# Kernel tuning notes

Measured on AMD Instinct MI355X. Metric: run time of the kernel, lower is better.

The kernel has to match this reference:

```python
import jax, jax.numpy as jnp
import numpy as np

D_MODEL = 1024
NHEAD = 16
HEAD_DIM = D_MODEL // NHEAD
SCALE = HEAD_DIM ** (-0.5)


def setup_inputs() -> dict:
    key = jax.random.key(0)
    k1, k2, k3 = jax.random.split(key, 3)
    B, T, C = 2, 2048, D_MODEL
    x = jax.random.normal(k1, (B, T, C), dtype=jnp.float32)
    W_qkv = jax.random.normal(k2, (3 * C, C), dtype=jnp.float32) * (C ** -0.5)
    b_qkv = jnp.zeros((3 * C,), dtype=jnp.float32)
    W_out = jax.random.normal(k3, (C, C), dtype=jnp.float32) * (C ** -0.5)
    b_out = jnp.zeros((C,), dtype=jnp.float32)
    return {"x": x, "W_qkv": W_qkv, "b_qkv": b_qkv, "W_out": W_out, "b_out": b_out}


def reference(x, W_qkv, b_qkv, W_out, b_out):
    B, T, C = x.shape
    H, hd = NHEAD, HEAD_DIM
    qkv = x @ W_qkv.T + b_qkv
    qkv = qkv.reshape(B, T, 3, H, hd).transpose(2, 0, 3, 1, 4)
    q, k, v = qkv[0], qkv[1], qkv[2]
    # scaled dot-product scores: (B,H,T,T)
    attn = jnp.einsum('bhqd,bhkd->bhqk', q, k) * SCALE
    # causal mask (is_causal=True): lower-triangular allowed
    causal = jnp.tril(jnp.ones((T, T), dtype=bool))
    attn = jnp.where(causal[None, None, :, :], attn, -jnp.inf)
    attn = jax.nn.softmax(attn, axis=-1)
    # (B,H,T,hd) -> (B,T,C)
    out = jnp.einsum('bhqk,bhkd->bhqd', attn, v)
    out = out.transpose(0, 2, 1, 3).reshape(B, T, C)
    out = out @ W_out.T + b_out
    return out
```

## Files before the change

### kernel.cpp

```cpp
#include <hip/hip_runtime.h>
#include <hip/hip_bf16.h>
#include <stdint.h>

#define D_MODEL 1024
#define NHEAD   16
#define HEAD_DIM 64
#define BATCH   2
#define SEQ     2048
#define M_TOK   (BATCH*SEQ)
#define N_QKV   (3*D_MODEL)
#define KDIM    1024
#define Q_SCALE (0.125f * 1.44269504088896f)

typedef __bf16 bf16_t;
typedef bf16_t bf16x8 __attribute__((ext_vector_type(8)));
typedef bf16_t bf16x4 __attribute__((ext_vector_type(4)));
typedef float  f32x4  __attribute__((ext_vector_type(4)));

__device__ __forceinline__ void gl_lds16(const void* g, void* l) {
    __builtin_amdgcn_global_load_lds(
        (__attribute__((address_space(1))) void*)(void*)(const_cast<void*>(g)),
        (__attribute__((address_space(3))) void*)l, 16, 0, 0);
}

#define N4_X  (M_TOK * KDIM / 4)
#define N4_W1 (N_QKV * KDIM / 4)
#define N4_W2 (D_MODEL * KDIM / 4)
__global__ void convert_all(const float* __restrict__ x,
                            const float* __restrict__ w1,
                            const float* __restrict__ w2,
                            bf16_t* __restrict__ ox,
                            bf16_t* __restrict__ o1,
                            bf16_t* __restrict__ o2) {
    int t = blockIdx.x * blockDim.x + threadIdx.x;
    const float* src;
    bf16_t* dst;
    int off;
    if (t < N4_X)                { src = x;  dst = ox; off = t; }
    else if (t < N4_X + N4_W1)   { src = w1; dst = o1; off = t - N4_X; }
    else                         { src = w2; dst = o2; off = t - N4_X - N4_W1; }
    float4 v = reinterpret_cast<const float4*>(src)[off];
    bf16x4 o = { (bf16_t)v.x, (bf16_t)v.y, (bf16_t)v.z, (bf16_t)v.w };
    reinterpret_cast<bf16x4*>(dst)[off] = o;
}

template <int MODE, int TN>
__global__ __launch_bounds__(256) void gemm_bt(
    const bf16_t* __restrict__ A,
    const bf16_t* __restrict__ Bw,
    const float*  __restrict__ bias,
    int N,
    bf16_t* __restrict__ qkv_out,
    bf16_t* __restrict__ vt_out,
    float*  __restrict__ f32_out)
{
    constexpr int NJ = TN / 32;
    __shared__ bf16_t As[128 * 64];
    __shared__ bf16_t Bs[TN * 64];

    const int cpx = gridDim.x >> 3;
    const int bid = (blockIdx.x & 7) * cpx + (blockIdx.x >> 3);

    const int nbn = N / TN;
    const int bm = bid / nbn;
    const int bn = bid % nbn;
    const int m0 = bm * 128, n0 = bn * TN;
    const int tid = threadIdx.x, wave = tid >> 6, lane = tid & 63;
    const int wr = wave >> 1, wc = wave & 1;

    f32x4 acc[4][NJ] = {};

    const int srow = lane >> 3;
    const int scol = ((lane & 7) ^ srow) * 8;
    const bf16_t* gA0 = A  + (size_t)(m0 + wave * 32 + srow) * KDIM + scol;
    const bf16_t* gB0 = Bw + (size_t)(n0 + wave * (TN / 4) + srow) * KDIM + scol;
    bf16_t* lA0 = &As[(wave * 32) * 64];
    bf16_t* lB0 = &Bs[(wave * (TN / 4)) * 64];

    const int fr = lane & 15;
    const int kq = lane >> 4;

    for (int k0 = 0; k0 < KDIM; k0 += 64) {
#pragma unroll
        for (int c = 0; c < 4; c++)
            gl_lds16(gA0 + (size_t)(c * 8) * KDIM + k0, lA0 + (c * 8) * 64);
#pragma unroll
        for (int c = 0; c < TN / 32; c++)
            gl_lds16(gB0 + (size_t)(c * 8) * KDIM + k0, lB0 + (c * 8) * 64);
        __syncthreads();

        bf16x8 af[2][4], bfr[2][NJ];
#pragma unroll
        for (int kk = 0; kk < 2; kk++) {
            const int ch = (((kk << 2) | kq) ^ (fr & 7)) * 8;
#pragma unroll
            for (int i = 0; i < 4; i++)
                af[kk][i] = *reinterpret_cast<const bf16x8*>(
                    &As[(wr * 64 + i * 16 + fr) * 64 + ch]);
#pragma unroll
            for (int j = 0; j < NJ; j++)
                bfr[kk][j] = *reinterpret_cast<const bf16x8*>(
                    &Bs[(wc * (TN / 2) + j * 16 + fr) * 64 + ch]);
        }
        __builtin_amdgcn_s_setprio(1);
#pragma unroll
        for (int i = 0; i < 4; i++)
#pragma unroll
            for (int j = 0; j < NJ; j++) {
                acc[i][j] = __builtin_amdgcn_mfma_f32_16x16x32_bf16(
                    af[0][i], bfr[0][j], acc[i][j], 0, 0, 0);
                acc[i][j] = __builtin_amdgcn_mfma_f32_16x16x32_bf16(
                    af[1][i], bfr[1][j], acc[i][j], 0, 0, 0);
            }
        __builtin_amdgcn_s_setprio(0);
        __syncthreads();
    }

#pragma unroll
    for (int i = 0; i < 4; i++) {
#pragma unroll
        for (int j = 0; j < NJ; j++) {
            const int col = n0 + wc * (TN / 2) + j * 16 + fr;
            const float bv = bias[col];
            const int row0 = m0 + wr * 64 + i * 16 + kq * 4;
            if (MODE == 1) {
#pragma unroll
                for (int r = 0; r < 4; r++)
                    f32_out[(size_t)(row0 + r) * N + col] = acc[i][j][r] + bv;
            } else if (col < 1024) {
#pragma unroll
                for (int r = 0; r < 4; r++)
                    qkv_out[(size_t)(row0 + r) * N_QKV + col] =
                        (bf16_t)((acc[i][j][r] + bv) * Q_SCALE);
            } else if (col < 2048) {
#pragma unroll
                for (int r = 0; r < 4; r++)
                    qkv_out[(size_t)(row0 + r) * N_QKV + col] =
                        (bf16_t)(acc[i][j][r] + bv);
            } else {
                const int d = col & 63, hh = (col >> 6) & 15;
                const int bb = row0 >> 11, t0 = row0 & 2047;
                bf16x4 pv = { (bf16_t)(acc[i][j][0] + bv),
                              (bf16_t)(acc[i][j][1] + bv),
                              (bf16_t)(acc[i][j][2] + bv),
                              (bf16_t)(acc[i][j][3] + bv) };
                *reinterpret_cast<bf16x4*>(
                    &vt_out[((size_t)((bb * NHEAD + hh) * HEAD_DIM + d)) * SEQ + t0]) = pv;
            }
        }
    }
}

__global__ __launch_bounds__(512) void attn_fwd(
    const bf16_t* __restrict__ qkv,
    const bf16_t* __restrict__ Vt,
    bf16_t* __restrict__ O)
{
    __shared__ bf16_t Ks[2][64 * 64];
    __shared__ bf16_t Vs[2][64 * 64];
    __shared__ bf16_t Ps[8][16 * 72];

    const int nqt = SEQ / 64;
    const int nbh = BATCH * NHEAD;
    const int qt = (nqt - 1) - (blockIdx.x / nbh);
    const int bh = blockIdx.x % nbh;
    const int b = bh >> 4, h = bh & 15;
    const int q0 = qt * 64;
    const int tid = threadIdx.x, wave = tid >> 6, lane = tid & 63;
    const int group = wave >> 2;
    const int w4 = wave & 3;
    const int fr = lane & 15;
    const int kq = lane >> 4;
    const int sw = fr & 7;
    const int c0 = (kq ^ sw) * 8;
    const int c1 = ((kq + 4) ^ sw) * 8;

    bf16x8 qf[2];
    {
        const size_t qrow = (size_t)(b * SEQ + q0 + w4 * 16 + fr);
        const int cbase = h * 64 + kq * 8;
        qf[0] = *reinterpret_cast<const bf16x8*>(&qkv[qrow * N_QKV + cbase]);
        qf[1] = *reinterpret_cast<const bf16x8*>(&qkv[qrow * N_QKV + cbase + 32]);
    }

    f32x4 acc_o[4] = {};
    float l_part = 0.f;

    const int srow = lane >> 3;
    const int scol = ((lane & 7) ^ srow) * 8;
    const bf16_t* gK = qkv + (size_t)(b * SEQ) * N_QKV + (D_MODEL + h * 64);
    const bf16_t* gV = Vt + (size_t)(bh * 64) * SEQ;

    const int nh0 = (qt + 2) >> 1;
    const int my_n = (group == 0) ? nh0 : (qt + 1 - nh0);
    const int base_t = (group == 0) ? 0 : nh0;

    for (int it = 0; it < nh0; ++it) {
        const bool act = (it < my_n);
        const int g_it = base_t + it;
        const int kv0 = g_it * 64;
        if (act) {
#pragma unroll
            for (int c = 0; c < 2; c++) {
                const int row = c * 32 + w4 * 8 + srow;
                gl_lds16(gK + (size_t)(kv0 + row) * N_QKV + scol,
                         &Ks[group][(c * 32 + w4 * 8) * 64]);
                gl_lds16(gV + (size_t)row * SEQ + kv0 + scol,
                         &Vs[group][(c * 32 + w4 * 8) * 64]);
            }
        }
        __syncthreads();

        if (act) {
            f32x4 s[4];
            __builtin_amdgcn_s_setprio(1);
#pragma unroll
            for (int j = 0; j < 4; j++) {
                bf16x8 k0f = *reinterpret_cast<const bf16x8*>(
                    &Ks[group][(j * 16 + fr) * 64 + c0]);
                bf16x8 k1f = *reinterpret_cast<const bf16x8*>(
                    &Ks[group][(j * 16 + fr) * 64 + c1]);
                f32x4 t = {0.f, 0.f, 0.f, 0.f};
                t = __builtin_amdgcn_mfma_f32_16x16x32_bf16(k0f, qf[0], t, 0, 0, 0);
                t = __builtin_amdgcn_mfma_f32_16x16x32_bf16(k1f, qf[1], t, 0, 0, 0);
                s[j] = t;
            }
            __builtin_amdgcn_s_setprio(0);

            if (g_it == qt) {
                const int qg = w4 * 16 + fr;
#pragma unroll
                for (int j = 0; j < 4; j++)
#pragma unroll
                    for (int r = 0; r < 4; r++)
                        if (j * 16 + kq * 4 + r > qg) s[j][r] = -1e30f;
            }

            float rs = 0.f;
#pragma unroll
            for (int j = 0; j < 4; j++)
#pragma unroll
                for (int r = 0; r < 4; r++) {
                    const float p = exp2f(s[j][r]);
                    s[j][r] = p;
                    rs += p;
                }
            l_part += rs;

#pragma unroll
            for (int j = 0; j < 4; j++) {
                bf16x4 pq = { (bf16_t)s[j][0], (bf16_t)s[j][1],
                              (bf16_t)s[j][2], (bf16_t)s[j][3] };
                *reinterpret_cast<bf16x4*>(&Ps[wave][fr * 72 + j * 16 + kq * 4]) = pq;
            }
            bf16x8 pb0 = *reinterpret_cast<const bf16x8*>(
                &Ps[wave][fr * 72 + kq * 8]);
            bf16x8 pb1 = *reinterpret_cast<const bf16x8*>(
                &Ps[wave][fr * 72 + 32 + kq * 8]);

            __builtin_amdgcn_s_setprio(1);
#pragma unroll
            for (int j = 0; j < 4; j++) {
                bf16x8 v0f = *reinterpret_cast<const bf16x8*>(
                    &Vs[group][(j * 16 + fr) * 64 + c0]);
                bf16x8 v1f = *reinterpret_cast<const bf16x8*>(
                    &Vs[group][(j * 16 + fr) * 64 + c1]);
                acc_o[j] = __builtin_amdgcn_mfma_f32_16x16x32_bf16(v0f, pb0, acc_o[j], 0, 0, 0);
                acc_o[j] = __builtin_amdgcn_mfma_f32_16x16x32_bf16(v1f, pb1, acc_o[j], 0, 0, 0);
            }
            __builtin_amdgcn_s_setprio(0);
        }

        __syncthreads();
    }

    float* Cf = reinterpret_cast<float*>(&Ps[0][0]);
    const int pbase = w4 * 1088;
    if (group == 1) {
#pragma unroll
        for (int j = 0; j < 4; j++)
#pragma unroll
            for (int r = 0; r < 4; r++)
                Cf[pbase + (j * 4 + r) * 64 + lane] = acc_o[j][r];
        Cf[pbase + 1024 + lane] = l_part;
    }
    __syncthreads();
    if (group == 0) {
#pragma unroll
        for (int j = 0; j < 4; j++)
#pragma unroll
            for (int r = 0; r < 4; r++)
                acc_o[j][r] += Cf[pbase + (j * 4 + r) * 64 + lane];
        l_part += Cf[pbase + 1024 + lane];

        l_part += __shfl_xor(l_part, 16);
        l_part += __shfl_xor(l_part, 32);
        const float inv = 1.0f / l_part;
        const size_t rowq = (size_t)(b * SEQ + q0 + w4 * 16 + fr);
#pragma unroll
        for (int j = 0; j < 4; j++) {
            bf16x4 ov = { (bf16_t)(acc_o[j][0] * inv), (bf16_t)(acc_o[j][1] * inv),
                          (bf16_t)(acc_o[j][2] * inv), (bf16_t)(acc_o[j][3] * inv) };
            *reinterpret_cast<bf16x4*>(&O[rowq * D_MODEL + h * 64 + j * 16 + kq * 4]) = ov;
        }
    }
}

extern "C" void kernel_launch(void* const* d_in, const int* in_sizes, int n_in,
                              void* d_out, int out_size, void* d_ws, size_t ws_size,
                              hipStream_t stream) {
    (void)in_sizes; (void)n_in; (void)out_size; (void)ws_size;
    const float* x    = (const float*)d_in[0];
    const float* Wqkv = (const float*)d_in[1];
    const float* bqkv = (const float*)d_in[2];
    const float* Wout = (const float*)d_in[3];
    const float* bout = (const float*)d_in[4];
    float* out = (float*)d_out;

    char* ws = (char*)d_ws;
    size_t off = 0;
    bf16_t* x_bf    = (bf16_t*)(ws + off); off += (size_t)M_TOK * KDIM * 2;
    bf16_t* wqkv_bf = (bf16_t*)(ws + off); off += (size_t)N_QKV * KDIM * 2;
    bf16_t* wout_bf = (bf16_t*)(ws + off); off += (size_t)D_MODEL * KDIM * 2;
    bf16_t* qkv     = (bf16_t*)(ws + off); off += (size_t)M_TOK * N_QKV * 2;
    bf16_t* vt      = (bf16_t*)(ws + off); off += (size_t)BATCH * NHEAD * HEAD_DIM * SEQ * 2;
    bf16_t* o_bf    = (bf16_t*)(ws + off); off += (size_t)M_TOK * D_MODEL * 2;

    convert_all<<<(N4_X + N4_W1 + N4_W2) / 256, 256, 0, stream>>>(
        x, Wqkv, Wout, x_bf, wqkv_bf, wout_bf);

    gemm_bt<0, 128><<<(M_TOK / 128) * (N_QKV / 128), 256, 0, stream>>>(
        x_bf, wqkv_bf, bqkv, N_QKV, qkv, vt, nullptr);

    attn_fwd<<<BATCH * NHEAD * (SEQ / 64), 512, 0, stream>>>(qkv, vt, o_bf);

    gemm_bt<1, 64><<<(M_TOK / 128) * (D_MODEL / 64), 256, 0, stream>>>(
        o_bf, wout_bf, bout, D_MODEL, nullptr, nullptr, out);
}
```

Baseline: 100.2 us.

## Use 32x32 MFMA in attention and keep P in registers

Rewrites the attention kernel to use 32x32x16 bf16 MFMA tiles with 4 waves (two groups of two) per block instead of 16x16x32 tiles with 8 waves. The score accumulator layout is arranged so that the exponentiated P values can be packed with v_cvt_pk_bf16_f32 and fed directly as the B operand of the PV MFMA. This removes the per-wave LDS round trip for P and its buffer. The cost is higher register pressure from 16-element accumulators and half as many waves per block, which may lower latency hiding.

```diff
diff --git a/kernel.cpp b/kernel.cpp
--- a/kernel.cpp
+++ b/kernel.cpp
@@ -16,11 +16,19 @@
 typedef bf16_t bf16x8 __attribute__((ext_vector_type(8)));
 typedef bf16_t bf16x4 __attribute__((ext_vector_type(4)));
 typedef float  f32x4  __attribute__((ext_vector_type(4)));
+typedef float  f32x16 __attribute__((ext_vector_type(16)));
+typedef unsigned u32x4 __attribute__((ext_vector_type(4)));
 
 __device__ __forceinline__ void gl_lds16(const void* g, void* l) {
     __builtin_amdgcn_global_load_lds(
         (__attribute__((address_space(1))) void*)(void*)(const_cast<void*>(g)),
         (__attribute__((address_space(3))) void*)l, 16, 0, 0);
+}
+
+__device__ __forceinline__ unsigned cvtpk_bf16(float a, float b) {
+    unsigned r;
+    asm("v_cvt_pk_bf16_f32 %0, %1, %2" : "=v"(r) : "v"(a), "v"(b));
+    return r;
 }
 
 #define N4_X  (M_TOK * KDIM / 4)
@@ -151,14 +159,13 @@
     }
 }
 
-__global__ __launch_bounds__(512) void attn_fwd(
+__global__ __launch_bounds__(256, 4) void attn_fwd(
     const bf16_t* __restrict__ qkv,
     const bf16_t* __restrict__ Vt,
     bf16_t* __restrict__ O)
 {
     __shared__ bf16_t Ks[2][64 * 64];
     __shared__ bf16_t Vs[2][64 * 64];
-    __shared__ bf16_t Ps[8][16 * 72];
 
     const int nqt = SEQ / 64;
     const int nbh = BATCH * NHEAD;
@@ -167,23 +174,23 @@
     const int b = bh >> 4, h = bh & 15;
     const int q0 = qt * 64;
     const int tid = threadIdx.x, wave = tid >> 6, lane = tid & 63;
-    const int group = wave >> 2;
-    const int w4 = wave & 3;
-    const int fr = lane & 15;
-    const int kq = lane >> 4;
-    const int sw = fr & 7;
-    const int c0 = (kq ^ sw) * 8;
-    const int c1 = ((kq + 4) ^ sw) * 8;
-
-    bf16x8 qf[2];
+    const int group = wave >> 1;
+    const int w4 = wave & 1;
+    const int ln31 = lane & 31;
+    const int ag = lane >> 5;
+    const int akey = ln31 & 7;
+
+    bf16x8 qf[4];
     {
-        const size_t qrow = (size_t)(b * SEQ + q0 + w4 * 16 + fr);
-        const int cbase = h * 64 + kq * 8;
-        qf[0] = *reinterpret_cast<const bf16x8*>(&qkv[qrow * N_QKV + cbase]);
-        qf[1] = *reinterpret_cast<const bf16x8*>(&qkv[qrow * N_QKV + cbase + 32]);
-    }
-
-    f32x4 acc_o[4] = {};
+        const size_t qrow = (size_t)(b * SEQ + q0 + w4 * 32 + ln31);
+        const bf16_t* qp = qkv + qrow * N_QKV + h * 64 + ag * 8;
+        qf[0] = *reinterpret_cast<const bf16x8*>(qp);
+        qf[1] = *reinterpret_cast<const bf16x8*>(qp + 16);
+        qf[2] = *reinterpret_cast<const bf16x8*>(qp + 32);
+        qf[3] = *reinterpret_cast<const bf16x8*>(qp + 48);
+    }
+
+    f32x16 acc[2] = {};
     float l_part = 0.f;
 
     const int srow = lane >> 3;
@@ -201,108 +208,113 @@
         const int kv0 = g_it * 64;
         if (act) {
 #pragma unroll
-            for (int c = 0; c < 2; c++) {
-                const int row = c * 32 + w4 * 8 + srow;
+            for (int c = 0; c < 4; c++) {
+                const int row = w4 * 32 + c * 8 + srow;
                 gl_lds16(gK + (size_t)(kv0 + row) * N_QKV + scol,
-                         &Ks[group][(c * 32 + w4 * 8) * 64]);
+                         &Ks[group][(w4 * 32 + c * 8) * 64]);
                 gl_lds16(gV + (size_t)row * SEQ + kv0 + scol,
-                         &Vs[group][(c * 32 + w4 * 8) * 64]);
+                         &Vs[group][(w4 * 32 + c * 8) * 64]);
             }
         }
         __syncthreads();
 
         if (act) {
-            f32x4 s[4];
-            __builtin_amdgcn_s_setprio(1);
-#pragma unroll
-            for (int j = 0; j < 4; j++) {
-                bf16x8 k0f = *reinterpret_cast<const bf16x8*>(
-                    &Ks[group][(j * 16 + fr) * 64 + c0]);
-                bf16x8 k1f = *reinterpret_cast<const bf16x8*>(
-                    &Ks[group][(j * 16 + fr) * 64 + c1]);
-                f32x4 t = {0.f, 0.f, 0.f, 0.f};
-                t = __builtin_amdgcn_mfma_f32_16x16x32_bf16(k0f, qf[0], t, 0, 0, 0);
-                t = __builtin_amdgcn_mfma_f32_16x16x32_bf16(k1f, qf[1], t, 0, 0, 0);
-                s[j] = t;
-            }
-            __builtin_amdgcn_s_setprio(0);
-
-            if (g_it == qt) {
-                const int qg = w4 * 16 + fr;
-#pragma unroll
-                for (int j = 0; j < 4; j++)
-#pragma unroll
-                    for (int r = 0; r < 4; r++)
-                        if (j * 16 + kq * 4 + r > qg) s[j][r] = -1e30f;
-            }
-
-            float rs = 0.f;
-#pragma unroll
-            for (int j = 0; j < 4; j++)
-#pragma unroll
-                for (int r = 0; r < 4; r++) {
-                    const float p = exp2f(s[j][r]);
-                    s[j][r] = p;
+#pragma unroll
+            for (int m = 0; m < 2; m++) {
+                f32x16 s = {};
+                __builtin_amdgcn_s_setprio(1);
+#pragma unroll
+                for (int c = 0; c < 4; c++) {
+                    bf16x8 kf = *reinterpret_cast<const bf16x8*>(
+                        &Ks[group][(m * 32 + ln31) * 64 + (((c * 2 + ag) ^ akey) * 8)]);
+                    s = __builtin_amdgcn_mfma_f32_32x32x16_bf16(kf, qf[c], s, 0, 0, 0);
+                }
+                __builtin_amdgcn_s_setprio(0);
+
+                if (g_it == qt) {
+                    const int qg = w4 * 32 + ln31;
+#pragma unroll
+                    for (int r = 0; r < 16; r++) {
+                        const int kvl = m * 32 + (r & 3) + 8 * (r >> 2) + 4 * ag;
+                        if (kvl > qg) s[r] = -1e30f;
+                    }
+                }
+
+                float rs = 0.f;
+#pragma unroll
+                for (int r = 0; r < 16; r++) {
+                    const float p = exp2f(s[r]);
+                    s[r] = p;
                     rs += p;
                 }
-            l_part += rs;
-
-#pragma unroll
-            for (int j = 0; j < 4; j++) {
-                bf16x4 pq = { (bf16_t)s[j][0], (bf16_t)s[j][1],
-                              (bf16_t)s[j][2], (bf16_t)s[j][3] };
-                *reinterpret_cast<bf16x4*>(&Ps[wave][fr * 72 + j * 16 + kq * 4]) = pq;
-            }
-            bf16x8 pb0 = *reinterpret_cast<const bf16x8*>(
-                &Ps[wave][fr * 72 + kq * 8]);
-            bf16x8 pb1 = *reinterpret_cast<const bf16x8*>(
-                &Ps[wave][fr * 72 + 32 + kq * 8]);
-
-            __builtin_amdgcn_s_setprio(1);
-#pragma unroll
-            for (int j = 0; j < 4; j++) {
-                bf16x8 v0f = *reinterpret_cast<const bf16x8*>(
-                    &Vs[group][(j * 16 + fr) * 64 + c0]);
-                bf16x8 v1f = *reinterpret_cast<const bf16x8*>(
-                    &Vs[group][(j * 16 + fr) * 64 + c1]);
-                acc_o[j] = __builtin_amdgcn_mfma_f32_16x16x32_bf16(v0f, pb0, acc_o[j], 0, 0, 0);
-                acc_o[j] = __builtin_amdgcn_mfma_f32_16x16x32_bf16(v1f, pb1, acc_o[j], 0, 0, 0);
-            }
-            __builtin_amdgcn_s_setprio(0);
+                l_part += rs;
+
+                __builtin_amdgcn_s_setprio(1);
+#pragma unroll
+                for (int c2 = 0; c2 < 2; c2++) {
+                    const int bs = c2 * 8;
+                    u32x4 bw = { cvtpk_bf16(s[bs + 0], s[bs + 1]),
+                                 cvtpk_bf16(s[bs + 2], s[bs + 3]),
+                                 cvtpk_bf16(s[bs + 4], s[bs + 5]),
+                                 cvtpk_bf16(s[bs + 6], s[bs + 7]) };
+                    bf16x8 pb = __builtin_bit_cast(bf16x8, bw);
+#pragma unroll
+                    for (int dm = 0; dm < 2; dm++) {
+                        const bf16_t* vrow = &Vs[group][(dm * 32 + ln31) * 64];
+                        const int Ca = 4 * m + 2 * c2;
+                        bf16x4 va = *reinterpret_cast<const bf16x4*>(
+                            &vrow[(Ca ^ akey) * 8 + ag * 4]);
+                        bf16x4 vb = *reinterpret_cast<const bf16x4*>(
+                            &vrow[((Ca + 1) ^ akey) * 8 + ag * 4]);
+                        bf16x8 vf;
+#pragma unroll
+                        for (int e = 0; e < 4; e++) {
+                            vf[e] = va[e];
+                            vf[4 + e] = vb[e];
+                        }
+                        acc[dm] = __builtin_amdgcn_mfma_f32_32x32x16_bf16(
+                            vf, pb, acc[dm], 0, 0, 0);
+                    }
+                }
+                __builtin_amdgcn_s_setprio(0);
+            }
         }
-
         __syncthreads();
     }
 
-    float* Cf = reinterpret_cast<float*>(&Ps[0][0]);
-    const int pbase = w4 * 1088;
+    float* Cf = reinterpret_cast<float*>(&Ks[0][0]);
+    const int cb = w4 * 2112;
     if (group == 1) {
 #pragma unroll
-        for (int j = 0; j < 4; j++)
-#pragma unroll
-            for (int r = 0; r < 4; r++)
-                Cf[pbase + (j * 4 + r) * 64 + lane] = acc_o[j][r];
-        Cf[pbase + 1024 + lane] = l_part;
+        for (int dm = 0; dm < 2; dm++)
+#pragma unroll
+            for (int r = 0; r < 16; r++)
+                Cf[cb + (dm * 16 + r) * 64 + lane] = acc[dm][r];
+        Cf[cb + 2048 + lane] = l_part;
     }
     __syncthreads();
     if (group == 0) {
 #pragma unroll
-        for (int j = 0; j < 4; j++)
-#pragma unroll
-            for (int r = 0; r < 4; r++)
-                acc_o[j][r] += Cf[pbase + (j * 4 + r) * 64 + lane];
-        l_part += Cf[pbase + 1024 + lane];
-
-        l_part += __shfl_xor(l_part, 16);
+        for (int dm = 0; dm < 2; dm++)
+#pragma unroll
+            for (int r = 0; r < 16; r++)
+                acc[dm][r] += Cf[cb + (dm * 16 + r) * 64 + lane];
+        l_part += Cf[cb + 2048 + lane];
+
         l_part += __shfl_xor(l_part, 32);
         const float inv = 1.0f / l_part;
-        const size_t rowq = (size_t)(b * SEQ + q0 + w4 * 16 + fr);
-#pragma unroll
-        for (int j = 0; j < 4; j++) {
-            bf16x4 ov = { (bf16_t)(acc_o[j][0] * inv), (bf16_t)(acc_o[j][1] * inv),
-                          (bf16_t)(acc_o[j][2] * inv), (bf16_t)(acc_o[j][3] * inv) };
-            *reinterpret_cast<bf16x4*>(&O[rowq * D_MODEL + h * 64 + j * 16 + kq * 4]) = ov;
-        }
+        const size_t rowq = (size_t)(b * SEQ + q0 + w4 * 32 + ln31);
+#pragma unroll
+        for (int dm = 0; dm < 2; dm++)
+#pragma unroll
+            for (int k = 0; k < 4; k++) {
+                const int d0 = dm * 32 + 8 * k + 4 * ag;
+                bf16x4 ov = { (bf16_t)(acc[dm][4 * k + 0] * inv),
+                              (bf16_t)(acc[dm][4 * k + 1] * inv),
+                              (bf16_t)(acc[dm][4 * k + 2] * inv),
+                              (bf16_t)(acc[dm][4 * k + 3] * inv) };
+                *reinterpret_cast<bf16x4*>(&O[rowq * D_MODEL + h * 64 + d0]) = ov;
+            }
     }
 }
 
@@ -332,7 +344,7 @@
     gemm_bt<0, 128><<<(M_TOK / 128) * (N_QKV / 128), 256, 0, stream>>>(
         x_bf, wqkv_bf, bqkv, N_QKV, qkv, vt, nullptr);
 
-    attn_fwd<<<BATCH * NHEAD * (SEQ / 64), 512, 0, stream>>>(qkv, vt, o_bf);
+    attn_fwd<<<BATCH * NHEAD * (SEQ / 64), 256, 0, stream>>>(qkv, vt, o_bf);
 
     gemm_bt<1, 64><<<(M_TOK / 128) * (D_MODEL / 64), 256, 0, stream>>>(
         o_bf, wout_bf, bout, D_MODEL, nullptr, nullptr, out);
```

Result: faster. 97.15 us (-3.0%).
